# Kernel tuning notes

Hardware: AMD Instinct MI355X
Metric: run time of the kernel (lower is better)

Reference implementation:

```python
import jax, jax.numpy as jnp
import numpy as np

SMOOTH = 1.0
IGNORE_INDEX = 255
NUM_CLASSES = 16


def setup_inputs() -> dict:
    key = jax.random.key(0)
    k1, k2 = jax.random.split(key)
    logits = jax.random.normal(k1, (8, NUM_CLASSES, 512, 512), dtype=jnp.float32)
    targets = jax.random.randint(k2, (8, 512, 512), 0, NUM_CLASSES, dtype=jnp.int64)
    return {"logits": logits, "targets": targets}


def reference(logits, targets):
    C = logits.shape[1]
    probs = jax.nn.softmax(logits, axis=1)  # [B,C,H,W]
    valid = (targets != IGNORE_INDEX)  # [B,H,W]
    t_safe = jnp.where(valid, targets, 0)
    # one-hot targets, zeroed at ignored pixels: [B,C,H,W]
    oh = jax.nn.one_hot(t_safe, C, axis=1, dtype=probs.dtype) * valid[:, None].astype(probs.dtype)
    # per-class reductions over batch + spatial dims
    intersection = jnp.sum(probs * oh, axis=(0, 2, 3))  # [C]
    p_sum = jnp.sum(probs, axis=(0, 2, 3))              # [C] (probs NOT masked, as in original)
    t_sum = jnp.sum(oh, axis=(0, 2, 3))                 # [C]
    dice = (2.0 * intersection + SMOOTH) / (p_sum + t_sum + SMOOTH)
    return jnp.mean(1.0 - dice)
```

## Files before the change

kernel.cpp:

```cpp
#include <hip/hip_runtime.h>

#define HW_  (512*512)
#define NC   16
#define NB   8
#define NPIX (NB*HW_)
#define NGRP (NPIX/4)
#define GPB  (HW_/4)


__global__ void dice_zero(float* ws) {
    int i = blockIdx.x * blockDim.x + threadIdx.x;
    if (i < 48) ws[i] = 0.0f;
}

__device__ __forceinline__ float wred(float v) {
    v += __shfl_xor(v, 32, 64);
    v += __shfl_xor(v, 16, 64);
    v += __shfl_xor(v,  8, 64);
    v += __shfl_xor(v,  4, 64);
    v += __shfl_xor(v,  2, 64);
    v += __shfl_xor(v,  1, 64);
    return v;
}

__global__ __launch_bounds__(256) void dice_main(
        const float* __restrict__ logits,
        const int*   __restrict__ targets,
        float*       __restrict__ ws) {
    float psum[NC], inter[NC], tsum[NC];
    #pragma unroll
    for (int c = 0; c < NC; ++c) { psum[c] = 0.f; inter[c] = 0.f; tsum[c] = 0.f; }

    const int nthreads = gridDim.x * blockDim.x;
    for (int g = blockIdx.x * blockDim.x + threadIdx.x; g < NGRP; g += nthreads) {
        const int b  = g >> 16;
        const int s4 = g & (GPB - 1);
        const float4* lp = reinterpret_cast<const float4*>(logits) + (size_t)b * (NC * GPB) + s4;
        const int4 t = reinterpret_cast<const int4*>(targets)[(size_t)b * GPB + s4];

        float4 e[NC];
        float sx = 0.f, sy = 0.f, sz = 0.f, sw = 0.f;
        #pragma unroll
        for (int c = 0; c < NC; ++c) {
            float4 l = lp[(size_t)c * GPB];
            e[c].x = __expf(l.x); e[c].y = __expf(l.y);
            e[c].z = __expf(l.z); e[c].w = __expf(l.w);
            sx += e[c].x; sy += e[c].y; sz += e[c].z; sw += e[c].w;
        }
        const float ix = __builtin_amdgcn_rcpf(sx);
        const float iy = __builtin_amdgcn_rcpf(sy);
        const float iz = __builtin_amdgcn_rcpf(sz);
        const float iw = __builtin_amdgcn_rcpf(sw);

        #pragma unroll
        for (int c = 0; c < NC; ++c) {
            const float px = e[c].x * ix, py = e[c].y * iy;
            const float pz = e[c].z * iz, pw = e[c].w * iw;
            psum[c] += (px + py) + (pz + pw);
            float ic = 0.f, tc = 0.f;
            if (t.x == c) { ic += px; tc += 1.f; }
            if (t.y == c) { ic += py; tc += 1.f; }
            if (t.z == c) { ic += pz; tc += 1.f; }
            if (t.w == c) { ic += pw; tc += 1.f; }
            inter[c] += ic;
            tsum[c]  += tc;
        }
    }

    __shared__ float red[4][48];
    const int lane = threadIdx.x & 63;
    const int wv   = threadIdx.x >> 6;
    #pragma unroll
    for (int c = 0; c < NC; ++c) {
        float a  = wred(psum[c]);
        float bb = wred(inter[c]);
        float cc = wred(tsum[c]);
        if (lane == 0) {
            red[wv][c]        = a;
            red[wv][NC + c]   = bb;
            red[wv][2*NC + c] = cc;
        }
    }
    __syncthreads();
    const int i = threadIdx.x;
    if (i < 48) {
        atomicAdd(&ws[i], red[0][i] + red[1][i] + red[2][i] + red[3][i]);
    }
}

__global__ void dice_final(const float* __restrict__ ws, float* __restrict__ out) {
    if (threadIdx.x == 0 && blockIdx.x == 0) {
        float acc = 0.f;
        #pragma unroll
        for (int c = 0; c < NC; ++c) {
            const float dice = (2.f * ws[NC + c] + 1.f) / (ws[c] + ws[2*NC + c] + 1.f);
            acc += 1.f - dice;
        }
        out[0] = acc * (1.f / 16.f);
    }
}

extern "C" void kernel_launch(void* const* d_in, const int* in_sizes, int n_in,
                              void* d_out, int out_size, void* d_ws, size_t ws_size,
                              hipStream_t stream) {
    const float* logits  = (const float*)d_in[0];
    const int*   targets = (const int*)d_in[1];
    float* ws  = (float*)d_ws;
    float* out = (float*)d_out;

    dice_zero<<<1, 64, 0, stream>>>(ws);
    dice_main<<<512, 256, 0, stream>>>(logits, targets, ws);
    dice_final<<<1, 64, 0, stream>>>(ws, out);
}
```

Measured before the change: 41.59 us.

## Gather target logit for intersection, pack target counts, fuse finalize via last-block

Replaces per-class compare chains for intersection and target counts with a direct gather of the target-class logit, accumulated through LDS atomics, and nibble-packed count registers. Switches to two pixels per thread with a fixed 1024-block grid and occupancy launch bounds. Spreads global atomics over 64 buckets and fuses the final dice computation into the last finishing block, removing the zero and final kernels in favour of a memset. This adds a redundant logit re-read and exp per pixel, plus LDS atomic contention.

```diff
diff --git a/kernel.cpp b/kernel.cpp
--- a/kernel.cpp
+++ b/kernel.cpp
@@ -1,17 +1,15 @@
 #include <hip/hip_runtime.h>
 
-#define HW_  (512*512)
-#define NC   16
-#define NB   8
-#define NPIX (NB*HW_)
-#define NGRP (NPIX/4)
-#define GPB  (HW_/4)
+#define HW_   (512*512)
+#define NC    16
+#define NB    8
+#define NPIX  (NB*HW_)
+#define GPB2  (HW_/2)
+#define NGRP2 (NPIX/2)
+#define NBLK  1024
+#define NTHR  256
+#define NBUK  64
 
-
-__global__ void dice_zero(float* ws) {
-    int i = blockIdx.x * blockDim.x + threadIdx.x;
-    if (i < 48) ws[i] = 0.0f;
-}
 
 __device__ __forceinline__ float wred(float v) {
     v += __shfl_xor(v, 32, 64);
@@ -23,80 +21,118 @@
     return v;
 }
 
-__global__ __launch_bounds__(256) void dice_main(
+__global__ __launch_bounds__(NTHR, 4) void dice_main(
         const float* __restrict__ logits,
         const int*   __restrict__ targets,
-        float*       __restrict__ ws) {
-    float psum[NC], inter[NC], tsum[NC];
+        float*       __restrict__ ws,
+        float*       __restrict__ out) {
+    __shared__ float lds_inter[NC];
+    __shared__ float red[4][2*NC];
+    __shared__ float fin[48];
+    __shared__ int   isLast;
+
+    const int tid = threadIdx.x;
+    if (tid < NC) lds_inter[tid] = 0.0f;
+    __syncthreads();
+
+    float psum[NC];
     #pragma unroll
-    for (int c = 0; c < NC; ++c) { psum[c] = 0.f; inter[c] = 0.f; tsum[c] = 0.f; }
+    for (int c = 0; c < NC; ++c) psum[c] = 0.0f;
+    unsigned tlo = 0u, thi = 0u;
 
-    const int nthreads = gridDim.x * blockDim.x;
-    for (int g = blockIdx.x * blockDim.x + threadIdx.x; g < NGRP; g += nthreads) {
-        const int b  = g >> 16;
-        const int s4 = g & (GPB - 1);
-        const float4* lp = reinterpret_cast<const float4*>(logits) + (size_t)b * (NC * GPB) + s4;
-        const int4 t = reinterpret_cast<const int4*>(targets)[(size_t)b * GPB + s4];
+    const float2* __restrict__ lf2 = reinterpret_cast<const float2*>(logits);
+    const int2*   __restrict__ tg2 = reinterpret_cast<const int2*>(targets);
 
-        float4 e[NC];
-        float sx = 0.f, sy = 0.f, sz = 0.f, sw = 0.f;
+    int g = blockIdx.x * NTHR + tid;
+    #pragma unroll 1
+    for (int k = 0; k < 4; ++k, g += NBLK * NTHR) {
+        const int b  = g >> 17;
+        const int s2 = g & (GPB2 - 1);
+        const float2* lp = lf2 + (size_t)b * (NC * GPB2) + s2;
+        const int2 t = tg2[(size_t)b * GPB2 + s2];
+
+        float ex[NC], ey[NC];
+        float sx = 0.0f, sy = 0.0f;
         #pragma unroll
         for (int c = 0; c < NC; ++c) {
-            float4 l = lp[(size_t)c * GPB];
-            e[c].x = __expf(l.x); e[c].y = __expf(l.y);
-            e[c].z = __expf(l.z); e[c].w = __expf(l.w);
-            sx += e[c].x; sy += e[c].y; sz += e[c].z; sw += e[c].w;
+            float2 l = lp[(size_t)c * GPB2];
+            ex[c] = __expf(l.x); ey[c] = __expf(l.y);
+            sx += ex[c]; sy += ey[c];
         }
         const float ix = __builtin_amdgcn_rcpf(sx);
         const float iy = __builtin_amdgcn_rcpf(sy);
-        const float iz = __builtin_amdgcn_rcpf(sz);
-        const float iw = __builtin_amdgcn_rcpf(sw);
 
         #pragma unroll
         for (int c = 0; c < NC; ++c) {
-            const float px = e[c].x * ix, py = e[c].y * iy;
-            const float pz = e[c].z * iz, pw = e[c].w * iw;
-            psum[c] += (px + py) + (pz + pw);
-            float ic = 0.f, tc = 0.f;
-            if (t.x == c) { ic += px; tc += 1.f; }
-            if (t.y == c) { ic += py; tc += 1.f; }
-            if (t.z == c) { ic += pz; tc += 1.f; }
-            if (t.w == c) { ic += pw; tc += 1.f; }
-            inter[c] += ic;
-            tsum[c]  += tc;
+            psum[c] = fmaf(ex[c], ix, psum[c]);
+            psum[c] = fmaf(ey[c], iy, psum[c]);
+        }
+
+        const float* lpx = logits + (size_t)b * (NC * HW_) + 2 * s2;
+        if ((unsigned)t.x < (unsigned)NC) {
+            const float pt = __expf(lpx[(size_t)t.x * HW_]) * ix;
+            atomicAdd(&lds_inter[t.x], pt);
+            const unsigned inc = 1u << (4 * (t.x & 7));
+            if (t.x < 8) tlo += inc; else thi += inc;
+        }
+        if ((unsigned)t.y < (unsigned)NC) {
+            const float pt = __expf(lpx[(size_t)t.y * HW_ + 1]) * iy;
+            atomicAdd(&lds_inter[t.y], pt);
+            const unsigned inc = 1u << (4 * (t.y & 7));
+            if (t.y < 8) tlo += inc; else thi += inc;
         }
     }
 
-    __shared__ float red[4][48];
-    const int lane = threadIdx.x & 63;
-    const int wv   = threadIdx.x >> 6;
+    const int lane = tid & 63, wv = tid >> 6;
     #pragma unroll
     for (int c = 0; c < NC; ++c) {
-        float a  = wred(psum[c]);
-        float bb = wred(inter[c]);
-        float cc = wred(tsum[c]);
-        if (lane == 0) {
-            red[wv][c]        = a;
-            red[wv][NC + c]   = bb;
-            red[wv][2*NC + c] = cc;
-        }
+        float r = wred(psum[c]);
+        if (lane == 0) red[wv][c] = r;
+    }
+    #pragma unroll
+    for (int c = 0; c < NC; ++c) {
+        float tc = (c < 8) ? (float)((tlo >> (4 * c)) & 15u)
+                           : (float)((thi >> (4 * (c - 8))) & 15u);
+        float r = wred(tc);
+        if (lane == 0) red[wv][NC + c] = r;
     }
     __syncthreads();
-    const int i = threadIdx.x;
-    if (i < 48) {
-        atomicAdd(&ws[i], red[0][i] + red[1][i] + red[2][i] + red[3][i]);
+
+    if (tid < 48) {
+        float v;
+        if (tid < 16)      v = red[0][tid] + red[1][tid] + red[2][tid] + red[3][tid];
+        else if (tid < 32) v = lds_inter[tid - 16];
+        else { const int c = tid - 32;
+               v = red[0][NC+c] + red[1][NC+c] + red[2][NC+c] + red[3][NC+c]; }
+        atomicAdd(&ws[(blockIdx.x & (NBUK - 1)) * 48 + tid], v);
+        __threadfence();
     }
-}
+    __syncthreads();
 
-__global__ void dice_final(const float* __restrict__ ws, float* __restrict__ out) {
-    if (threadIdx.x == 0 && blockIdx.x == 0) {
-        float acc = 0.f;
+    if (tid == 0) {
+        int old = atomicAdd((int*)(ws + NBUK * 48), 1);
+        isLast = (old == (int)gridDim.x - 1);
+    }
+    __syncthreads();
+    if (!isLast) return;
+
+    __threadfence();
+    if (tid < 48) {
+        float s = 0.0f;
+        #pragma unroll 8
+        for (int b2 = 0; b2 < NBUK; ++b2)
+            s += atomicAdd(&ws[b2 * 48 + tid], 0.0f);
+        fin[tid] = s;
+    }
+    __syncthreads();
+    if (tid == 0) {
+        float acc = 0.0f;
         #pragma unroll
         for (int c = 0; c < NC; ++c) {
-            const float dice = (2.f * ws[NC + c] + 1.f) / (ws[c] + ws[2*NC + c] + 1.f);
-            acc += 1.f - dice;
+            const float dice = (2.0f * fin[16 + c] + 1.0f) / (fin[c] + fin[32 + c] + 1.0f);
+            acc += 1.0f - dice;
         }
-        out[0] = acc * (1.f / 16.f);
+        out[0] = acc * (1.0f / 16.0f);
     }
 }
 
@@ -108,7 +144,6 @@
     float* ws  = (float*)d_ws;
     float* out = (float*)d_out;
 
-    dice_zero<<<1, 64, 0, stream>>>(ws);
-    dice_main<<<512, 256, 0, stream>>>(logits, targets, ws);
-    dice_final<<<1, 64, 0, stream>>>(ws, out);
+    hipMemsetAsync(ws, 0, 16384, stream);
+    dice_main<<<NBLK, NTHR, 0, stream>>>(logits, targets, ws, out);
 }
```

After: 62.28 us. 1.5x slower.

## Fuse finalize into main kernel with last-block counter and bucketed atomics

Applied to the files above, without the earlier changes.

Launches one thread per pixel group across 2048 blocks instead of a grid-stride loop, reduces per-class sums per block into 16 atomic buckets, and has the last block to finish compute the final dice loss. The separate zero and finalize kernels are replaced by a memset and the in-kernel tail. This removes one launch and atomic contention but performs the full wave reduction per pixel group rather than once per thread, raising shuffle work.

```diff
diff --git a/kernel.cpp b/kernel.cpp
--- a/kernel.cpp
+++ b/kernel.cpp
@@ -1,17 +1,12 @@
 #include <hip/hip_runtime.h>
 
-#define HW_  (512*512)
-#define NC   16
-#define NB   8
-#define NPIX (NB*HW_)
-#define NGRP (NPIX/4)
-#define GPB  (HW_/4)
+#define HW_   (512*512)
+#define NC    16
+#define GPB4  (HW_/4)
+#define NBLK  2048
+#define NTHR  256
+#define NBUK  16
 
-
-__global__ void dice_zero(float* ws) {
-    int i = blockIdx.x * blockDim.x + threadIdx.x;
-    if (i < 48) ws[i] = 0.0f;
-}
 
 __device__ __forceinline__ float wred(float v) {
     v += __shfl_xor(v, 32, 64);
@@ -23,77 +18,82 @@
     return v;
 }
 
-__global__ __launch_bounds__(256) void dice_main(
+__global__ __launch_bounds__(NTHR, 4) void dice_main(
         const float* __restrict__ logits,
         const int*   __restrict__ targets,
-        float*       __restrict__ ws) {
-    float psum[NC], inter[NC], tsum[NC];
-    #pragma unroll
-    for (int c = 0; c < NC; ++c) { psum[c] = 0.f; inter[c] = 0.f; tsum[c] = 0.f; }
+        float*       __restrict__ ws,
+        float*       __restrict__ out) {
+    __shared__ float red[4][48];
+    __shared__ float fin[48];
+    __shared__ int   isLast;
 
-    const int nthreads = gridDim.x * blockDim.x;
-    for (int g = blockIdx.x * blockDim.x + threadIdx.x; g < NGRP; g += nthreads) {
-        const int b  = g >> 16;
-        const int s4 = g & (GPB - 1);
-        const float4* lp = reinterpret_cast<const float4*>(logits) + (size_t)b * (NC * GPB) + s4;
-        const int4 t = reinterpret_cast<const int4*>(targets)[(size_t)b * GPB + s4];
+    const int tid = threadIdx.x;
+    const int g   = blockIdx.x * NTHR + tid;
+    const int b   = g >> 16;
+    const int s4  = g & (GPB4 - 1);
 
-        float4 e[NC];
-        float sx = 0.f, sy = 0.f, sz = 0.f, sw = 0.f;
-        #pragma unroll
-        for (int c = 0; c < NC; ++c) {
-            float4 l = lp[(size_t)c * GPB];
-            e[c].x = __expf(l.x); e[c].y = __expf(l.y);
-            e[c].z = __expf(l.z); e[c].w = __expf(l.w);
-            sx += e[c].x; sy += e[c].y; sz += e[c].z; sw += e[c].w;
-        }
-        const float ix = __builtin_amdgcn_rcpf(sx);
-        const float iy = __builtin_amdgcn_rcpf(sy);
-        const float iz = __builtin_amdgcn_rcpf(sz);
-        const float iw = __builtin_amdgcn_rcpf(sw);
+    const float4* lp = reinterpret_cast<const float4*>(logits) + (size_t)b * (NC * GPB4) + s4;
+    const int4 t = reinterpret_cast<const int4*>(targets)[(size_t)b * GPB4 + s4];
 
-        #pragma unroll
-        for (int c = 0; c < NC; ++c) {
-            const float px = e[c].x * ix, py = e[c].y * iy;
-            const float pz = e[c].z * iz, pw = e[c].w * iw;
-            psum[c] += (px + py) + (pz + pw);
-            float ic = 0.f, tc = 0.f;
-            if (t.x == c) { ic += px; tc += 1.f; }
-            if (t.y == c) { ic += py; tc += 1.f; }
-            if (t.z == c) { ic += pz; tc += 1.f; }
-            if (t.w == c) { ic += pw; tc += 1.f; }
-            inter[c] += ic;
-            tsum[c]  += tc;
-        }
-    }
-
-    __shared__ float red[4][48];
-    const int lane = threadIdx.x & 63;
-    const int wv   = threadIdx.x >> 6;
+    float4 e[NC];
+    float sx = 0.f, sy = 0.f, sz = 0.f, sw = 0.f;
     #pragma unroll
     for (int c = 0; c < NC; ++c) {
-        float a  = wred(psum[c]);
-        float bb = wred(inter[c]);
-        float cc = wred(tsum[c]);
-        if (lane == 0) {
-            red[wv][c]        = a;
-            red[wv][NC + c]   = bb;
-            red[wv][2*NC + c] = cc;
-        }
+        const float4 l = lp[(size_t)c * GPB4];
+        e[c].x = __expf(l.x); e[c].y = __expf(l.y);
+        e[c].z = __expf(l.z); e[c].w = __expf(l.w);
+        sx += e[c].x; sy += e[c].y; sz += e[c].z; sw += e[c].w;
+    }
+    const float ix = __builtin_amdgcn_rcpf(sx);
+    const float iy = __builtin_amdgcn_rcpf(sy);
+    const float iz = __builtin_amdgcn_rcpf(sz);
+    const float iw = __builtin_amdgcn_rcpf(sw);
+
+    const int lane = tid & 63, wv = tid >> 6;
+    #pragma unroll
+    for (int c = 0; c < NC; ++c) {
+        const float px = e[c].x * ix, py = e[c].y * iy;
+        const float pz = e[c].z * iz, pw = e[c].w * iw;
+        const float ps = (px + py) + (pz + pw);
+        const float ic = (t.x == c ? px : 0.f) + (t.y == c ? py : 0.f)
+                       + (t.z == c ? pz : 0.f) + (t.w == c ? pw : 0.f);
+        const float tc = (t.x == c ? 1.f : 0.f) + (t.y == c ? 1.f : 0.f)
+                       + (t.z == c ? 1.f : 0.f) + (t.w == c ? 1.f : 0.f);
+        const float rp = wred(ps);
+        const float ri = wred(ic);
+        const float rt = wred(tc);
+        if (lane == 0) { red[wv][c] = rp; red[wv][16 + c] = ri; red[wv][32 + c] = rt; }
     }
     __syncthreads();
-    const int i = threadIdx.x;
-    if (i < 48) {
-        atomicAdd(&ws[i], red[0][i] + red[1][i] + red[2][i] + red[3][i]);
+
+    if (tid < 48) {
+        const float v = red[0][tid] + red[1][tid] + red[2][tid] + red[3][tid];
+        atomicAdd(&ws[(blockIdx.x & (NBUK - 1)) * 48 + tid], v);
+        __threadfence();
     }
-}
+    __syncthreads();
 
-__global__ void dice_final(const float* __restrict__ ws, float* __restrict__ out) {
-    if (threadIdx.x == 0 && blockIdx.x == 0) {
+    if (tid == 0) {
+        const int old = atomicAdd((int*)(ws + NBUK * 48), 1);
+        isLast = (old == NBLK - 1);
+    }
+    __syncthreads();
+    if (!isLast) return;
+
+    __threadfence();
+    if (tid < 48) {
+        float s = 0.f;
+        #pragma unroll
+        for (int k = 0; k < NBUK; ++k)
+            s += atomicAdd(&ws[k * 48 + tid], 0.0f);
+        fin[tid] = s;
+    }
+    __syncthreads();
+    if (tid == 0) {
         float acc = 0.f;
         #pragma unroll
         for (int c = 0; c < NC; ++c) {
-            const float dice = (2.f * ws[NC + c] + 1.f) / (ws[c] + ws[2*NC + c] + 1.f);
+            const float dice = (2.f * fin[16 + c] + 1.f) / (fin[c] + fin[32 + c] + 1.f);
             acc += 1.f - dice;
         }
         out[0] = acc * (1.f / 16.f);
@@ -108,7 +108,6 @@
     float* ws  = (float*)d_ws;
     float* out = (float*)d_out;
 
-    dice_zero<<<1, 64, 0, stream>>>(ws);
-    dice_main<<<512, 256, 0, stream>>>(logits, targets, ws);
-    dice_final<<<1, 64, 0, stream>>>(ws, out);
+    hipMemsetAsync(ws, 0, 4096, stream);
+    dice_main<<<NBLK, NTHR, 0, stream>>>(logits, targets, ws, out);
 }
```

New measurement: 88.10 us. +111.8%, slower.
